# Kernel optimization log

Measured on AMD Instinct MI355X. Metric: run time of the kernel, lower is better.

## Reference

```python
import jax, jax.numpy as jnp
import numpy as np

N_NODES = 50000
N_EDGES = 1600000
IN_FEATS = 128
HIDDEN = 32
HEADS = 4
N_GRAPHS = 64
NEG_SLOPE = 0.2


def setup_inputs() -> dict:
    key = jax.random.key(0)
    ks = jax.random.split(key, 10)
    features = jax.random.normal(ks[0], (N_NODES, IN_FEATS), dtype=jnp.float32)
    src = jax.random.randint(ks[1], (N_EDGES,), 0, N_NODES, dtype=jnp.int32)
    dst = jax.random.randint(ks[2], (N_EDGES,), 0, N_NODES, dtype=jnp.int32)
    graph_ids = jnp.sort(jax.random.randint(ks[3], (N_NODES,), 0, N_GRAPHS, dtype=jnp.int32))
    # GATConv params (fc has no bias in DGL; conv bias added post-aggregation)
    s = 1.0 / np.sqrt(IN_FEATS)
    W = jax.random.uniform(ks[4], (IN_FEATS, HEADS * HIDDEN), jnp.float32, -s, s)
    attn_l = jax.random.normal(ks[5], (HEADS, HIDDEN), dtype=jnp.float32) * 0.1
    attn_r = jax.random.normal(ks[6], (HEADS, HIDDEN), dtype=jnp.float32) * 0.1
    bias = jnp.zeros((HEADS * HIDDEN,), dtype=jnp.float32)
    s2 = 1.0 / np.sqrt(HEADS * HIDDEN)
    fc_w = jax.random.uniform(ks[7], (HEADS * HIDDEN, 1), jnp.float32, -s2, s2)
    fc_b = jnp.zeros((1,), dtype=jnp.float32)
    return dict(features=features, src=src, dst=dst, graph_ids=graph_ids,
                W=W, attn_l=attn_l, attn_r=attn_r, bias=bias, fc_w=fc_w, fc_b=fc_b)


def reference(features, src, dst, graph_ids, W, attn_l, attn_r, bias, fc_w, fc_b):
    N = features.shape[0]
    H, D = attn_l.shape
    feat = (features @ W).reshape(N, H, D)              # [N,H,D]
    el = jnp.sum(feat * attn_l[None], axis=-1)          # [N,H]
    er = jnp.sum(feat * attn_r[None], axis=-1)          # [N,H]
    e = jax.nn.leaky_relu(el[src] + er[dst], NEG_SLOPE) # [E,H]
    # edge softmax over incoming edges of each dst node
    m = jax.ops.segment_max(e, dst, num_segments=N)     # [N,H]
    ex = jnp.exp(e - m[dst])
    denom = jax.ops.segment_sum(ex, dst, num_segments=N)
    a = ex / denom[dst]                                 # [E,H]
    msg = feat[src] * a[:, :, None]                     # [E,H,D]
    rst = jax.ops.segment_sum(msg, dst, num_segments=N) # [N,H,D]
    h = rst.reshape(N, H * D) + bias[None, :]
    # dropout(p=0.5) treated as identity (eval mode)
    h = jax.nn.elu(h)
    counts = jax.ops.segment_sum(jnp.ones((N,), h.dtype), graph_ids, num_segments=N_GRAPHS)
    hg = jax.ops.segment_sum(h, graph_ids, num_segments=N_GRAPHS) / counts[:, None]
    y = jax.nn.sigmoid(hg @ fc_w + fc_b[None, :])       # [G,1]
    return y
```

## Files before the change

kernel.cpp:

```cpp
#include <hip/hip_runtime.h>
#include <hip/hip_bf16.h>
#include <math.h>

#define N_NODES 50000
#define N_EDGES 1600000
#define HEADS 4
#define HIDDEN 32
#define N_GRAPHS 64
#define NEG_SLOPE 0.2f

#define NBUCK 196
#define BKT_EPT 8
#define BKT_CHUNK (256 * BKT_EPT)
#define NBKB ((N_EDGES + BKT_CHUNK - 1) / BKT_CHUNK)

#define OFS_FEAT 0
#define OFS_EBUF 0
#define OFS_EL   6400000
#define OFS_ER   6600000
#define OFS_P    6800000
#define OFS_GCNT 6850000
#define OFS_GBASE 6850256
#define OFS_GPOS 6850512
#define OFS_OFF  6900000
#define OFS_SRC  6950272

#define GLD16(g, l)                                                            \
  __builtin_amdgcn_global_load_lds(                                            \
      (const __attribute__((address_space(1))) void*)(g),                      \
      (__attribute__((address_space(3))) void*)(l), 16, 0, 0)

__device__ __forceinline__ unsigned pack_bf16x2(float a, float b) {
  __hip_bfloat16 ha = __float2bfloat16(a), hb = __float2bfloat16(b);
  unsigned ua = *(const unsigned short*)&ha, ub = *(const unsigned short*)&hb;
  return ua | (ub << 16);
}
__device__ __forceinline__ float bf16_lo(unsigned u) {
  unsigned v = u << 16; return *(const float*)&v;
}
__device__ __forceinline__ float bf16_hi(unsigned u) {
  unsigned v = u & 0xFFFF0000u; return *(const float*)&v;
}

#define FMA4(A, XS, WV)                                                        \
  A.x = fmaf(XS, WV.x, A.x);                                                   \
  A.y = fmaf(XS, WV.y, A.y);                                                   \
  A.z = fmaf(XS, WV.z, A.z);                                                   \
  A.w = fmaf(XS, WV.w, A.w);

#define DOT4(A, B) ((A).x * (B).x + (A).y * (B).y + (A).z * (B).z + (A).w * (B).w)

__global__ __launch_bounds__(256, 2) void k_gemm(
    const float* __restrict__ X, const float* __restrict__ W,
    const float* __restrict__ attn_l, const float* __restrict__ attn_r,
    unsigned* __restrict__ featb, float* __restrict__ el, float* __restrict__ er) {
  __shared__ float Wl[128 * 128];
  __shared__ float Xl[32 * 128];
  const int t = threadIdx.x;
  const int lane = t & 63;
  const int wave = t >> 6;

  for (int i = 0; i < 16; ++i) {
    int chunk = i * 4 + wave;
    GLD16(W + chunk * 256 + lane * 4, Wl + chunk * 256);
  }

  const int u = t & 31;
  const int gn = t >> 5;
  const int h = u >> 3;
  const float4 al = *(const float4*)&attn_l[h * 32 + 4 * (u & 7)];
  const float4 ar = *(const float4*)&attn_r[h * 32 + 4 * (u & 7)];
  const int ntiles = (N_NODES + 31) / 32;
  __syncthreads();

  for (int tile = blockIdx.x; tile < ntiles; tile += gridDim.x) {
    const int n0 = tile * 32;
    if (n0 + 32 <= N_NODES) {
      for (int i = 0; i < 4; ++i) {
        int chunk = i * 4 + wave;
        GLD16(X + n0 * 128 + chunk * 256 + lane * 4, Xl + chunk * 256);
      }
    } else {
      for (int i = t; i < 1024; i += 256) {
        int row = i >> 5, kq = i & 31;
        float4 v = make_float4(0.f, 0.f, 0.f, 0.f);
        if (n0 + row < N_NODES)
          v = ((const float4*)(X + (size_t)(n0 + row) * 128))[kq];
        ((float4*)Xl)[i] = v;
      }
    }
    __syncthreads();

    float4 a0 = make_float4(0.f, 0.f, 0.f, 0.f);
    float4 a1 = a0, a2 = a0, a3 = a0;
#pragma unroll 4
    for (int k = 0; k < 128; k += 4) {
      float4 w0 = *(const float4*)&Wl[(k + 0) * 128 + 4 * u];
      float4 w1 = *(const float4*)&Wl[(k + 1) * 128 + 4 * u];
      float4 w2 = *(const float4*)&Wl[(k + 2) * 128 + 4 * u];
      float4 w3 = *(const float4*)&Wl[(k + 3) * 128 + 4 * u];
      float4 x0 = *(const float4*)&Xl[(gn * 4 + 0) * 128 + k];
      float4 x1 = *(const float4*)&Xl[(gn * 4 + 1) * 128 + k];
      float4 x2 = *(const float4*)&Xl[(gn * 4 + 2) * 128 + k];
      float4 x3 = *(const float4*)&Xl[(gn * 4 + 3) * 128 + k];
      FMA4(a0, x0.x, w0) FMA4(a0, x0.y, w1) FMA4(a0, x0.z, w2) FMA4(a0, x0.w, w3)
      FMA4(a1, x1.x, w0) FMA4(a1, x1.y, w1) FMA4(a1, x1.z, w2) FMA4(a1, x1.w, w3)
      FMA4(a2, x2.x, w0) FMA4(a2, x2.y, w1) FMA4(a2, x2.z, w2) FMA4(a2, x2.w, w3)
      FMA4(a3, x3.x, w0) FMA4(a3, x3.y, w1) FMA4(a3, x3.z, w2) FMA4(a3, x3.w, w3)
    }
    const int nb = n0 + gn * 4;
    if (nb + 0 < N_NODES)
      *(uint2*)&featb[(size_t)(nb + 0) * 64 + 2 * u] =
          make_uint2(pack_bf16x2(a0.x, a0.y), pack_bf16x2(a0.z, a0.w));
    if (nb + 1 < N_NODES)
      *(uint2*)&featb[(size_t)(nb + 1) * 64 + 2 * u] =
          make_uint2(pack_bf16x2(a1.x, a1.y), pack_bf16x2(a1.z, a1.w));
    if (nb + 2 < N_NODES)
      *(uint2*)&featb[(size_t)(nb + 2) * 64 + 2 * u] =
          make_uint2(pack_bf16x2(a2.x, a2.y), pack_bf16x2(a2.z, a2.w));
    if (nb + 3 < N_NODES)
      *(uint2*)&featb[(size_t)(nb + 3) * 64 + 2 * u] =
          make_uint2(pack_bf16x2(a3.x, a3.y), pack_bf16x2(a3.z, a3.w));

    float pl0 = DOT4(a0, al), pl1 = DOT4(a1, al), pl2 = DOT4(a2, al), pl3 = DOT4(a3, al);
    float pr0 = DOT4(a0, ar), pr1 = DOT4(a1, ar), pr2 = DOT4(a2, ar), pr3 = DOT4(a3, ar);
#pragma unroll
    for (int m = 1; m < 8; m <<= 1) {
      pl0 += __shfl_xor(pl0, m, 64); pl1 += __shfl_xor(pl1, m, 64);
      pl2 += __shfl_xor(pl2, m, 64); pl3 += __shfl_xor(pl3, m, 64);
      pr0 += __shfl_xor(pr0, m, 64); pr1 += __shfl_xor(pr1, m, 64);
      pr2 += __shfl_xor(pr2, m, 64); pr3 += __shfl_xor(pr3, m, 64);
    }
    if ((u & 7) == 0) {
      if (nb + 0 < N_NODES) { el[(nb + 0) * 4 + h] = pl0; er[(nb + 0) * 4 + h] = pr0; }
      if (nb + 1 < N_NODES) { el[(nb + 1) * 4 + h] = pl1; er[(nb + 1) * 4 + h] = pr1; }
      if (nb + 2 < N_NODES) { el[(nb + 2) * 4 + h] = pl2; er[(nb + 2) * 4 + h] = pr2; }
      if (nb + 3 < N_NODES) { el[(nb + 3) * 4 + h] = pl3; er[(nb + 3) * 4 + h] = pr3; }
    }
    __syncthreads();
  }
}

__global__ void k_bhist(const int* __restrict__ dst, int* __restrict__ gcount) {
  __shared__ int lh[NBUCK];
  const int t = threadIdx.x;
  if (t < NBUCK) lh[t] = 0;
  __syncthreads();
  const int base = blockIdx.x * BKT_CHUNK;
#pragma unroll
  for (int j = 0; j < BKT_EPT; ++j) {
    int e = base + j * 256 + t;
    if (e < N_EDGES) atomicAdd(&lh[dst[e] >> 8], 1);
  }
  __syncthreads();
  if (t < NBUCK && lh[t] > 0) atomicAdd(&gcount[t], lh[t]);
}

__global__ void k_bscan(const int* __restrict__ gcount, int* __restrict__ gbase,
                        int* __restrict__ gpos) {
  __shared__ int sh[256];
  const int t = threadIdx.x;
  int v = (t < NBUCK) ? gcount[t] : 0;
  sh[t] = v;
  __syncthreads();
  for (int s = 1; s < 256; s <<= 1) {
    int add = (t >= s) ? sh[t - s] : 0;
    __syncthreads();
    sh[t] += add;
    __syncthreads();
  }
  int excl = sh[t] - v;
  if (t < NBUCK) { gbase[t] = excl; gpos[t] = excl; }
  if (t == NBUCK - 1) gbase[NBUCK] = excl + v;
}

__global__ void k_bucket(const int* __restrict__ src, const int* __restrict__ dst,
                         int* __restrict__ gpos, int2* __restrict__ ebuf) {
  __shared__ int lh[NBUCK];
  __shared__ int lbase[NBUCK];
  const int t = threadIdx.x;
  if (t < NBUCK) lh[t] = 0;
  __syncthreads();
  const int base = blockIdx.x * BKT_CHUNK;
  int s8[BKT_EPT], d8[BKT_EPT], r8[BKT_EPT], b8[BKT_EPT];
#pragma unroll
  for (int j = 0; j < BKT_EPT; ++j) {
    int e = base + j * 256 + t;
    bool ok = e < N_EDGES;
    s8[j] = ok ? src[e] : 0;
    d8[j] = ok ? dst[e] : 0;
    b8[j] = d8[j] >> 8;
    int r = 0;
    if (ok) r = atomicAdd(&lh[b8[j]], 1);
    r8[j] = r;
  }
  __syncthreads();
  if (t < NBUCK && lh[t] > 0) lbase[t] = atomicAdd(&gpos[t], lh[t]);
  __syncthreads();
#pragma unroll
  for (int j = 0; j < BKT_EPT; ++j) {
    int e = base + j * 256 + t;
    if (e < N_EDGES) ebuf[lbase[b8[j]] + r8[j]] = make_int2(s8[j], d8[j]);
  }
}

__global__ __launch_bounds__(1024) void k_bsort(
    const int2* __restrict__ ebuf, const int* __restrict__ gbase,
    int* __restrict__ srcbuf, int* __restrict__ off) {
  __shared__ int lcnt[256];
  __shared__ int loff[256];
  __shared__ int lpos[256];
  const int t = threadIdx.x;
  const int b = blockIdx.x;
  const int lo = gbase[b], hi = gbase[b + 1];
  if (t < 256) lcnt[t] = 0;
  __syncthreads();
  for (int i = lo + t; i < hi; i += 1024)
    atomicAdd(&lcnt[ebuf[i].y & 255], 1);
  __syncthreads();
  int v = (t < 256) ? lcnt[t] : 0;
  if (t < 256) loff[t] = v;
  __syncthreads();
  for (int s = 1; s < 256; s <<= 1) {
    int add = (t >= s && t < 256) ? loff[t - s] : 0;
    __syncthreads();
    if (t < 256) loff[t] += add;
    __syncthreads();
  }
  if (t < 256) {
    int excl = loff[t] - v;
    lpos[t] = excl;
    int node = b * 256 + t;
    if (node < N_NODES) off[node] = lo + excl;
  }
  if (b == NBUCK - 1 && t == 0) off[N_NODES] = N_EDGES;
  __syncthreads();
  for (int i = lo + t; i < hi; i += 1024) {
    int2 e = ebuf[i];
    int p = atomicAdd(&lpos[e.y & 255], 1);
    srcbuf[lo + p] = e.x;
  }
}

__global__ __launch_bounds__(256) void k_aggregate(
    const unsigned* __restrict__ featb, const float* __restrict__ el,
    const float* __restrict__ er, const int* __restrict__ off,
    const int* __restrict__ srcbuf, const float* __restrict__ bias,
    const float* __restrict__ fc_w, float* __restrict__ pbuf) {
  int gid = blockIdx.x * blockDim.x + threadIdx.x;
  int v = gid >> 6;
  if (v >= N_NODES) return;
  const int lane = threadIdx.x & 63;
  const int sub = lane & 15;
  const int par = lane >> 4;
  const int h = sub >> 2;

  const float erv = er[v * 4 + h];
  const int start = off[v], end = off[v + 1];

  float sum = 0.f;
  float acc0 = 0.f, acc1 = 0.f, acc2 = 0.f, acc3 = 0.f;
  float acc4 = 0.f, acc5 = 0.f, acc6 = 0.f, acc7 = 0.f;

  int iA = start + par;
  if (iA < end) {
    int sA = srcbuf[iA];
    float eA = el[sA * 4 + h];
    uint4 fA = *(const uint4*)&featb[(size_t)sA * 64 + sub * 4];

    int iB = iA + 4;
    bool hasB = iB < end;
    float eB = 0.f; uint4 fB = make_uint4(0, 0, 0, 0);
    if (hasB) {
      int sB = srcbuf[iB];
      eB = el[sB * 4 + h];
      fB = *(const uint4*)&featb[(size_t)sB * 64 + sub * 4];
    }

    while (true) {
      const int iC = iB + 4;
      const bool hasC = iC < end;
      float eC = 0.f; uint4 fC = make_uint4(0, 0, 0, 0);
      if (hasC) {
        int sC = srcbuf[iC];
        eC = el[sC * 4 + h];
        fC = *(const uint4*)&featb[(size_t)sC * 64 + sub * 4];
      }

      float e = eA + erv;
      e = (e > 0.f) ? e : NEG_SLOPE * e;
      float p = __expf(e);
      sum += p;
      acc0 = fmaf(bf16_lo(fA.x), p, acc0);
      acc1 = fmaf(bf16_hi(fA.x), p, acc1);
      acc2 = fmaf(bf16_lo(fA.y), p, acc2);
      acc3 = fmaf(bf16_hi(fA.y), p, acc3);
      acc4 = fmaf(bf16_lo(fA.z), p, acc4);
      acc5 = fmaf(bf16_hi(fA.z), p, acc5);
      acc6 = fmaf(bf16_lo(fA.w), p, acc6);
      acc7 = fmaf(bf16_hi(fA.w), p, acc7);

      if (!hasB) break;
      eA = eB; fA = fB;
      iB = iC; hasB = hasC; eB = eC; fB = fC;
    }
  }

#pragma unroll
  for (int mk = 16; mk < 64; mk <<= 1) {
    sum += __shfl_xor(sum, mk, 64);
    acc0 += __shfl_xor(acc0, mk, 64);
    acc1 += __shfl_xor(acc1, mk, 64);
    acc2 += __shfl_xor(acc2, mk, 64);
    acc3 += __shfl_xor(acc3, mk, 64);
    acc4 += __shfl_xor(acc4, mk, 64);
    acc5 += __shfl_xor(acc5, mk, 64);
    acc6 += __shfl_xor(acc6, mk, 64);
    acc7 += __shfl_xor(acc7, mk, 64);
  }

  const float inv = (end > start) ? 1.f / sum : 0.f;
  const float4 b4a = *(const float4*)&bias[sub * 8];
  const float4 b4b = *(const float4*)&bias[sub * 8 + 4];
  const float4 w4a = *(const float4*)&fc_w[sub * 8];
  const float4 w4b = *(const float4*)&fc_w[sub * 8 + 4];
  float r0 = fmaf(acc0, inv, b4a.x);
  float r1 = fmaf(acc1, inv, b4a.y);
  float r2 = fmaf(acc2, inv, b4a.z);
  float r3 = fmaf(acc3, inv, b4a.w);
  float r4 = fmaf(acc4, inv, b4b.x);
  float r5 = fmaf(acc5, inv, b4b.y);
  float r6 = fmaf(acc6, inv, b4b.z);
  float r7 = fmaf(acc7, inv, b4b.w);
  r0 = (r0 > 0.f) ? r0 : __expf(r0) - 1.f;
  r1 = (r1 > 0.f) ? r1 : __expf(r1) - 1.f;
  r2 = (r2 > 0.f) ? r2 : __expf(r2) - 1.f;
  r3 = (r3 > 0.f) ? r3 : __expf(r3) - 1.f;
  r4 = (r4 > 0.f) ? r4 : __expf(r4) - 1.f;
  r5 = (r5 > 0.f) ? r5 : __expf(r5) - 1.f;
  r6 = (r6 > 0.f) ? r6 : __expf(r6) - 1.f;
  r7 = (r7 > 0.f) ? r7 : __expf(r7) - 1.f;
  float t = r0 * w4a.x + r1 * w4a.y + r2 * w4a.z + r3 * w4a.w +
            r4 * w4b.x + r5 * w4b.y + r6 * w4b.z + r7 * w4b.w;
#pragma unroll
  for (int mk = 1; mk < 16; mk <<= 1) t += __shfl_xor(t, mk, 64);
  if (lane == 0) pbuf[v] = t;
}

__global__ void k_pool(const float* __restrict__ pbuf, const int* __restrict__ gids,
                       const float* __restrict__ fc_b, float* __restrict__ y) {
  int g = blockIdx.x;
  int a = 0, b = N_NODES;
  while (a < b) { int mid = (a + b) >> 1; if (gids[mid] < g) a = mid + 1; else b = mid; }
  int lo = a;
  b = N_NODES;
  while (a < b) { int mid = (a + b) >> 1; if (gids[mid] < g + 1) a = mid + 1; else b = mid; }
  int hi = a;

  float s = 0.f;
  for (int i = lo + threadIdx.x; i < hi; i += blockDim.x) s += pbuf[i];
  __shared__ float sh[256];
  sh[threadIdx.x] = s;
  __syncthreads();
  for (int st = 128; st > 0; st >>= 1) {
    if (threadIdx.x < st) sh[threadIdx.x] += sh[threadIdx.x + st];
    __syncthreads();
  }
  if (threadIdx.x == 0) {
    float cnt = (float)(hi - lo);
    float hg = sh[0] / cnt;
    float x = hg + fc_b[0];
    y[g] = 1.f / (1.f + expf(-x));
  }
}

extern "C" void kernel_launch(void* const* d_in, const int* in_sizes, int n_in,
                              void* d_out, int out_size, void* d_ws, size_t ws_size,
                              hipStream_t stream) {
  const float* features = (const float*)d_in[0];
  const int* src = (const int*)d_in[1];
  const int* dst = (const int*)d_in[2];
  const int* gids = (const int*)d_in[3];
  const float* W = (const float*)d_in[4];
  const float* attn_l = (const float*)d_in[5];
  const float* attn_r = (const float*)d_in[6];
  const float* bias = (const float*)d_in[7];
  const float* fc_w = (const float*)d_in[8];
  const float* fc_b = (const float*)d_in[9];

  float* ws = (float*)d_ws;
  unsigned* featb = (unsigned*)d_ws + OFS_FEAT;
  int2* ebuf = (int2*)((int*)d_ws + OFS_EBUF);
  float* el = ws + OFS_EL;
  float* er = ws + OFS_ER;
  float* pbuf = ws + OFS_P;
  int* gcount = (int*)d_ws + OFS_GCNT;
  int* gbase = (int*)d_ws + OFS_GBASE;
  int* gpos = (int*)d_ws + OFS_GPOS;
  int* off = (int*)d_ws + OFS_OFF;
  int* srcbuf = (int*)d_ws + OFS_SRC;

  hipMemsetAsync(gcount, 0, NBUCK * sizeof(int), stream);

  k_bhist<<<NBKB, 256, 0, stream>>>(dst, gcount);
  k_bscan<<<1, 256, 0, stream>>>(gcount, gbase, gpos);
  k_bucket<<<NBKB, 256, 0, stream>>>(src, dst, gpos, ebuf);
  k_bsort<<<NBUCK, 1024, 0, stream>>>(ebuf, gbase, srcbuf, off);

  k_gemm<<<512, 256, 0, stream>>>(features, W, attn_l, attn_r, featb, el, er);

  k_aggregate<<<(N_NODES * 64) / 256 + 1, 256, 0, stream>>>(featb, el, er, off, srcbuf,
                                                            bias, fc_w, pbuf);
  k_pool<<<N_GRAPHS, 256, 0, stream>>>(pbuf, gids, fc_b, (float*)d_out);
}
```

Baseline: 253.7 us.

## Rewrite projection GEMM with bf16 MFMA and fold attention vectors into weights

The FP32 FMA projection GEMM is replaced by a bf16 MFMA 16x16x32 kernel over 64-node tiles. A new small kernel precomputes W·attn_l and W·attn_r as 8 extra weight columns, so el/er come out of the same MFMA pass instead of shuffle reductions. Inputs and weights are converted to bf16 in padded LDS, which lowers precision of el/er and features. Each block now reloads and converts all of W from global, adding per-block setup cost.

```diff
diff --git a/kernel.cpp b/kernel.cpp
--- a/kernel.cpp
+++ b/kernel.cpp
@@ -22,13 +22,14 @@
 #define OFS_GCNT 6850000
 #define OFS_GBASE 6850256
 #define OFS_GPOS 6850512
+#define OFS_WAB  6850768
 #define OFS_OFF  6900000
 #define OFS_SRC  6950272
 
-#define GLD16(g, l)                                                            \
-  __builtin_amdgcn_global_load_lds(                                            \
-      (const __attribute__((address_space(1))) void*)(g),                      \
-      (__attribute__((address_space(3))) void*)(l), 16, 0, 0)
+typedef __attribute__((ext_vector_type(8))) short short8;
+typedef __attribute__((ext_vector_type(4))) float f32x4;
+
+#define LDS_S 68
 
 __device__ __forceinline__ unsigned pack_bf16x2(float a, float b) {
   __hip_bfloat16 ha = __float2bfloat16(a), hb = __float2bfloat16(b);
@@ -42,102 +43,104 @@
   unsigned v = u & 0xFFFF0000u; return *(const float*)&v;
 }
 
-#define FMA4(A, XS, WV)                                                        \
-  A.x = fmaf(XS, WV.x, A.x);                                                   \
-  A.y = fmaf(XS, WV.y, A.y);                                                   \
-  A.z = fmaf(XS, WV.z, A.z);                                                   \
-  A.w = fmaf(XS, WV.w, A.w);
-
-#define DOT4(A, B) ((A).x * (B).x + (A).y * (B).y + (A).z * (B).z + (A).w * (B).w)
+__global__ __launch_bounds__(1024) void k_wab(const float* __restrict__ W,
+                                              const float* __restrict__ al,
+                                              const float* __restrict__ ar,
+                                              float* __restrict__ wab) {
+  int t = threadIdx.x;
+  int k = t >> 3, c = t & 7;
+  int h = c & 3;
+  const float* av = (c < 4) ? al : ar;
+  float s = 0.f;
+  for (int d = 0; d < 32; ++d)
+    s = fmaf(W[k * 128 + h * 32 + d], av[h * 32 + d], s);
+  wab[k * 8 + c] = s;
+}
 
 __global__ __launch_bounds__(256, 2) void k_gemm(
     const float* __restrict__ X, const float* __restrict__ W,
-    const float* __restrict__ attn_l, const float* __restrict__ attn_r,
-    unsigned* __restrict__ featb, float* __restrict__ el, float* __restrict__ er) {
-  __shared__ float Wl[128 * 128];
-  __shared__ float Xl[32 * 128];
+    const float* __restrict__ wab, unsigned* __restrict__ featb,
+    float* __restrict__ el, float* __restrict__ er) {
+  __shared__ unsigned Wt[144 * LDS_S];
+  __shared__ unsigned Xt[64 * LDS_S];
   const int t = threadIdx.x;
   const int lane = t & 63;
-  const int wave = t >> 6;
-
-  for (int i = 0; i < 16; ++i) {
-    int chunk = i * 4 + wave;
-    GLD16(W + chunk * 256 + lane * 4, Wl + chunk * 256);
-  }
-
-  const int u = t & 31;
-  const int gn = t >> 5;
-  const int h = u >> 3;
-  const float4 al = *(const float4*)&attn_l[h * 32 + 4 * (u & 7)];
-  const float4 ar = *(const float4*)&attn_r[h * 32 + 4 * (u & 7)];
-  const int ntiles = (N_NODES + 31) / 32;
-  __syncthreads();
-
-  for (int tile = blockIdx.x; tile < ntiles; tile += gridDim.x) {
-    const int n0 = tile * 32;
-    if (n0 + 32 <= N_NODES) {
-      for (int i = 0; i < 4; ++i) {
-        int chunk = i * 4 + wave;
-        GLD16(X + n0 * 128 + chunk * 256 + lane * 4, Xl + chunk * 256);
+  const int wv = t >> 6;
+  const int nb0 = blockIdx.x * 64;
+
+  {
+    const int c = t & 127;
+    const int ph = (t >> 7) * 32;
+    for (int p = ph; p < ph + 32; ++p)
+      Wt[c * LDS_S + p] = pack_bf16x2(W[(2 * p) * 128 + c], W[(2 * p + 1) * 128 + c]);
+  }
+  if (t < 128) {
+    const int c = t & 7;
+    const int p0 = (t >> 3) * 4;
+    for (int q = 0; q < 4; ++q) {
+      int p = p0 + q;
+      Wt[(128 + c) * LDS_S + p] =
+          pack_bf16x2(wab[(2 * p) * 8 + c], wab[(2 * p + 1) * 8 + c]);
+    }
+  } else {
+    const int c = (t - 128) & 7;
+    const int p0 = ((t - 128) >> 3) * 4;
+    for (int q = 0; q < 4; ++q) Wt[(136 + c) * LDS_S + p0 + q] = 0;
+  }
+  {
+    const int row = t >> 2;
+    const int c0 = (t & 3) * 32;
+    const int node = nb0 + row;
+    const float4* xs = (const float4*)(X + (size_t)node * 128 + c0);
+    for (int i = 0; i < 8; ++i) {
+      float4 v = make_float4(0.f, 0.f, 0.f, 0.f);
+      if (node < N_NODES) v = xs[i];
+      int p = (c0 >> 1) + i * 2;
+      Xt[row * LDS_S + p] = pack_bf16x2(v.x, v.y);
+      Xt[row * LDS_S + p + 1] = pack_bf16x2(v.z, v.w);
+    }
+  }
+  __syncthreads();
+
+  const int rrow = lane & 15;
+  const int rgrp = lane >> 4;
+  f32x4 acc[9];
+#pragma unroll
+  for (int i = 0; i < 9; ++i) acc[i] = (f32x4){0.f, 0.f, 0.f, 0.f};
+  const int arow = wv * 16 + rrow;
+
+#pragma unroll
+  for (int kk = 0; kk < 4; ++kk) {
+    const int pbase = kk * 16 + rgrp * 4;
+    short8 afrag = *(const short8*)&Xt[arow * LDS_S + pbase];
+#pragma unroll
+    for (int bt = 0; bt < 9; ++bt) {
+      short8 bfrag = *(const short8*)&Wt[(bt * 16 + rrow) * LDS_S + pbase];
+      acc[bt] = __builtin_amdgcn_mfma_f32_16x16x32_bf16(afrag, bfrag, acc[bt], 0, 0, 0);
+    }
+  }
+
+  const int nodebase = nb0 + wv * 16 + rgrp * 4;
+#pragma unroll
+  for (int bt = 0; bt < 8; ++bt) {
+#pragma unroll
+    for (int j = 0; j < 4; ++j) {
+      float other = __shfl_xor(acc[bt][j], 1, 64);
+      if ((lane & 1) == 0) {
+        int node = nodebase + j;
+        if (node < N_NODES)
+          featb[(size_t)node * 64 + bt * 8 + (rrow >> 1)] =
+              pack_bf16x2(acc[bt][j], other);
       }
-    } else {
-      for (int i = t; i < 1024; i += 256) {
-        int row = i >> 5, kq = i & 31;
-        float4 v = make_float4(0.f, 0.f, 0.f, 0.f);
-        if (n0 + row < N_NODES)
-          v = ((const float4*)(X + (size_t)(n0 + row) * 128))[kq];
-        ((float4*)Xl)[i] = v;
-      }
-    }
-    __syncthreads();
-
-    float4 a0 = make_float4(0.f, 0.f, 0.f, 0.f);
-    float4 a1 = a0, a2 = a0, a3 = a0;
-#pragma unroll 4
-    for (int k = 0; k < 128; k += 4) {
-      float4 w0 = *(const float4*)&Wl[(k + 0) * 128 + 4 * u];
-      float4 w1 = *(const float4*)&Wl[(k + 1) * 128 + 4 * u];
-      float4 w2 = *(const float4*)&Wl[(k + 2) * 128 + 4 * u];
-      float4 w3 = *(const float4*)&Wl[(k + 3) * 128 + 4 * u];
-      float4 x0 = *(const float4*)&Xl[(gn * 4 + 0) * 128 + k];
-      float4 x1 = *(const float4*)&Xl[(gn * 4 + 1) * 128 + k];
-      float4 x2 = *(const float4*)&Xl[(gn * 4 + 2) * 128 + k];
-      float4 x3 = *(const float4*)&Xl[(gn * 4 + 3) * 128 + k];
-      FMA4(a0, x0.x, w0) FMA4(a0, x0.y, w1) FMA4(a0, x0.z, w2) FMA4(a0, x0.w, w3)
-      FMA4(a1, x1.x, w0) FMA4(a1, x1.y, w1) FMA4(a1, x1.z, w2) FMA4(a1, x1.w, w3)
-      FMA4(a2, x2.x, w0) FMA4(a2, x2.y, w1) FMA4(a2, x2.z, w2) FMA4(a2, x2.w, w3)
-      FMA4(a3, x3.x, w0) FMA4(a3, x3.y, w1) FMA4(a3, x3.z, w2) FMA4(a3, x3.w, w3)
-    }
-    const int nb = n0 + gn * 4;
-    if (nb + 0 < N_NODES)
-      *(uint2*)&featb[(size_t)(nb + 0) * 64 + 2 * u] =
-          make_uint2(pack_bf16x2(a0.x, a0.y), pack_bf16x2(a0.z, a0.w));
-    if (nb + 1 < N_NODES)
-      *(uint2*)&featb[(size_t)(nb + 1) * 64 + 2 * u] =
-          make_uint2(pack_bf16x2(a1.x, a1.y), pack_bf16x2(a1.z, a1.w));
-    if (nb + 2 < N_NODES)
-      *(uint2*)&featb[(size_t)(nb + 2) * 64 + 2 * u] =
-          make_uint2(pack_bf16x2(a2.x, a2.y), pack_bf16x2(a2.z, a2.w));
-    if (nb + 3 < N_NODES)
-      *(uint2*)&featb[(size_t)(nb + 3) * 64 + 2 * u] =
-          make_uint2(pack_bf16x2(a3.x, a3.y), pack_bf16x2(a3.z, a3.w));
-
-    float pl0 = DOT4(a0, al), pl1 = DOT4(a1, al), pl2 = DOT4(a2, al), pl3 = DOT4(a3, al);
-    float pr0 = DOT4(a0, ar), pr1 = DOT4(a1, ar), pr2 = DOT4(a2, ar), pr3 = DOT4(a3, ar);
-#pragma unroll
-    for (int m = 1; m < 8; m <<= 1) {
-      pl0 += __shfl_xor(pl0, m, 64); pl1 += __shfl_xor(pl1, m, 64);
-      pl2 += __shfl_xor(pl2, m, 64); pl3 += __shfl_xor(pl3, m, 64);
-      pr0 += __shfl_xor(pr0, m, 64); pr1 += __shfl_xor(pr1, m, 64);
-      pr2 += __shfl_xor(pr2, m, 64); pr3 += __shfl_xor(pr3, m, 64);
-    }
-    if ((u & 7) == 0) {
-      if (nb + 0 < N_NODES) { el[(nb + 0) * 4 + h] = pl0; er[(nb + 0) * 4 + h] = pr0; }
-      if (nb + 1 < N_NODES) { el[(nb + 1) * 4 + h] = pl1; er[(nb + 1) * 4 + h] = pr1; }
-      if (nb + 2 < N_NODES) { el[(nb + 2) * 4 + h] = pl2; er[(nb + 2) * 4 + h] = pr2; }
-      if (nb + 3 < N_NODES) { el[(nb + 3) * 4 + h] = pl3; er[(nb + 3) * 4 + h] = pr3; }
-    }
-    __syncthreads();
+    }
+  }
+#pragma unroll
+  for (int j = 0; j < 4; ++j) {
+    int node = nodebase + j;
+    if (node < N_NODES) {
+      if (rrow < 4) el[node * 4 + rrow] = acc[8][j];
+      else if (rrow < 8) er[node * 4 + (rrow - 4)] = acc[8][j];
+    }
   }
 }
 
@@ -397,17 +400,20 @@
   int* gcount = (int*)d_ws + OFS_GCNT;
   int* gbase = (int*)d_ws + OFS_GBASE;
   int* gpos = (int*)d_ws + OFS_GPOS;
+  float* wab = ws + OFS_WAB;
   int* off = (int*)d_ws + OFS_OFF;
   int* srcbuf = (int*)d_ws + OFS_SRC;
 
   hipMemsetAsync(gcount, 0, NBUCK * sizeof(int), stream);
+
+  k_wab<<<1, 1024, 0, stream>>>(W, attn_l, attn_r, wab);
 
   k_bhist<<<NBKB, 256, 0, stream>>>(dst, gcount);
   k_bscan<<<1, 256, 0, stream>>>(gcount, gbase, gpos);
   k_bucket<<<NBKB, 256, 0, stream>>>(src, dst, gpos, ebuf);
   k_bsort<<<NBUCK, 1024, 0, stream>>>(ebuf, gbase, srcbuf, off);
 
-  k_gemm<<<512, 256, 0, stream>>>(features, W, attn_l, attn_r, featb, el, er);
+  k_gemm<<<(N_NODES + 63) / 64, 256, 0, stream>>>(features, W, wab, featb, el, er);
 
   k_aggregate<<<(N_NODES * 64) / 256 + 1, 256, 0, stream>>>(featb, el, er, off, srcbuf,
                                                             bias, fc_w, pbuf);
```

After: 244.1 us. -3.8%, faster.
